# Kernel tuning notes

Measured on AMD Instinct MI355X. Metric: run time of the kernel, lower is better.

The kernel has to match this reference:

```python
import jax, jax.numpy as jnp
import numpy as np

EPS = 1e-8
B, N, W, H = 64, 8192, 64, 4
CTRL = H * (W + 1 + 1 + 3 + 1)  # 280


def setup_inputs() -> dict:
    key = jax.random.key(0)
    k1, k2, k3 = jax.random.split(key, 3)
    memory = jax.random.normal(k1, (B, N, W), dtype=jnp.float32)
    controls = jax.random.normal(k2, (B, CTRL), dtype=jnp.float32)
    prev_weights = jax.random.uniform(k3, (B, H, N), dtype=jnp.float32)
    prev_weights = prev_weights / prev_weights.sum(-1, keepdims=True)
    return {"memory": memory, "controls": controls, "prev_weights": prev_weights}


def reference(memory, controls, prev_weights):
    # memory: [B, N, W]; controls: [B, H*(W+6)]; prev_weights: [B, H, N]
    b, n, w = memory.shape
    h = prev_weights.shape[1]
    # split controls per input_partition = [W, 1, 1, 3, 1] per head
    pos = 0
    keys = controls[:, pos:pos + h * w].reshape(b, h, w); pos += h * w
    betas = controls[:, pos:pos + h].reshape(b, h, 1); pos += h
    gates = controls[:, pos:pos + h].reshape(b, h, 1); pos += h
    shifts = controls[:, pos:pos + 3 * h].reshape(b, h, 3); pos += 3 * h
    gammas = controls[:, pos:pos + h].reshape(b, h, 1)

    keys = jnp.tanh(keys)
    betas = jax.nn.softplus(betas)
    gates = jax.nn.sigmoid(gates)
    shifts = jax.nn.softmax(shifts, axis=-1)
    gammas = 1.0 + jax.nn.softplus(gammas)

    # cosine-similarity content addressing: [B, H, N]
    dots = jnp.einsum('bnw,bhw->bhn', memory, keys)
    norm = (jnp.linalg.norm(keys, axis=-1)[:, :, None]
            * jnp.linalg.norm(memory, axis=-1)[:, None, :])
    scores = dots / (norm + EPS) * betas
    w_content = jax.nn.softmax(scores, axis=-1)

    # interpolate with previous weights
    w_interp = gates * w_content + (1.0 - gates) * prev_weights

    # circular convolution with 3-tap shift kernel (torch conv2d = correlation):
    # out[i] = s0*w[i-1] + s1*w[i] + s2*w[i+1] (indices mod N)
    w_shift = (shifts[..., 0:1] * jnp.roll(w_interp, 1, axis=-1)
               + shifts[..., 1:2] * w_interp
               + shifts[..., 2:3] * jnp.roll(w_interp, -1, axis=-1))

    # sharpen and renormalize
    w_sharp = w_shift ** gammas
    w_sharp = w_sharp / (w_sharp.sum(-1, keepdims=True) + EPS)

    # read: [B, H, W]
    read_data = jnp.einsum('bnw,bhn->bhw', memory, w_sharp)
    return read_data
```

## Files before the change

### kernel.cpp

```cpp
#include <hip/hip_runtime.h>
#include <math.h>

#define B_ 64
#define N_ 8192
#define W_ 64
#define H_ 4
#define CTRL_ 280
#define EPS_ 1e-8f

__device__ __forceinline__ float softplusf(float x) {
    return fmaxf(x, 0.f) + log1pf(expf(-fabsf(x)));
}

__device__ __forceinline__ float waveReduceSum(float v) {
    #pragma unroll
    for (int m = 1; m < 64; m <<= 1) v += __shfl_xor(v, m, 64);
    return v;
}

template <int NW>
__device__ __forceinline__ float blockReduceSum(float v, float* scr) {
    int t = threadIdx.x;
    v = waveReduceSum(v);
    if ((t & 63) == 0) scr[t >> 6] = v;
    __syncthreads();
    float r = 0.f;
    #pragma unroll
    for (int i = 0; i < NW; ++i) r += scr[i];
    __syncthreads();
    return r;
}

__global__ __launch_bounds__(256) void k_scores(const float* __restrict__ mem,
                                                const float* __restrict__ ctrl,
                                                float* __restrict__ expsc) {
    __shared__ float keys[H_ * 68];
    __shared__ float knorm[H_];
    __shared__ float beta[H_];
    __shared__ float sstage[H_ * 65];

    const int t  = threadIdx.x;
    const int b  = blockIdx.y;
    const int n0 = blockIdx.x * 64;

    {
        int h = t >> 6, w = t & 63;
        float kv = tanhf(ctrl[b * CTRL_ + h * W_ + w]);
        keys[h * 68 + w] = kv;
        float ss = waveReduceSum(kv * kv);
        if (w == 0) knorm[h] = sqrtf(ss);
        if (t < H_) beta[t] = softplusf(ctrl[b * CTRL_ + H_ * W_ + t]);
    }
    __syncthreads();

    {
        int row = t >> 2, h = t & 3;
        const float4* mrow = reinterpret_cast<const float4*>(
            mem + ((size_t)b * N_ + n0 + row) * W_);
        const float4* krow = reinterpret_cast<const float4*>(&keys[h * 68]);
        float dot = 0.f, ss = 0.f;
        #pragma unroll
        for (int wg = 0; wg < 16; ++wg) {
            float4 mv = mrow[wg];
            float4 kv = krow[wg];
            dot += mv.x * kv.x + mv.y * kv.y + mv.z * kv.z + mv.w * kv.w;
            ss  += mv.x * mv.x + mv.y * mv.y + mv.z * mv.z + mv.w * mv.w;
        }
        float bh_ = beta[h];
        float sc = dot / (sqrtf(ss) * knorm[h] + EPS_) * bh_;
        sstage[h * 65 + row] = expf(sc - bh_);
    }
    __syncthreads();

    {
        int h = t >> 6, r = t & 63;
        expsc[((size_t)(b * H_ + h)) * N_ + n0 + r] = sstage[h * 65 + r];
    }
}

__global__ __launch_bounds__(512) void k_weights(const float* __restrict__ expsc,
                                                 const float* __restrict__ ctrl,
                                                 const float* __restrict__ prev,
                                                 float* __restrict__ wnorm,
                                                 float* __restrict__ out) {
    __shared__ float scr[8];
    __shared__ float firsts[512];
    __shared__ float lasts[512];

    const int t  = threadIdx.x;
    const int bh = blockIdx.x;
    const int b  = bh >> 2;
    const int h  = bh & 3;

    if (t < 16) {
        float4 z = {0.f, 0.f, 0.f, 0.f};
        reinterpret_cast<float4*>(out + (size_t)bh * 64)[t] = z;
    }

    const float4* sp = reinterpret_cast<const float4*>(expsc + (size_t)bh * N_) + t * 4;
    float a[16];
    float eloc = 0.f;
    #pragma unroll
    for (int i = 0; i < 4; ++i) {
        float4 v = sp[i];
        a[i * 4 + 0] = v.x; a[i * 4 + 1] = v.y; a[i * 4 + 2] = v.z; a[i * 4 + 3] = v.w;
        eloc += v.x + v.y + v.z + v.w;
    }
    float L = blockReduceSum<8>(eloc, scr);
    float invL = 1.f / L;

    const float* cb = ctrl + b * CTRL_;
    float g  = 1.f / (1.f + expf(-cb[260 + h]));
    float r0 = cb[264 + 3 * h], r1 = cb[265 + 3 * h], r2 = cb[266 + 3 * h];
    float rm = fmaxf(r0, fmaxf(r1, r2));
    float e0 = expf(r0 - rm), e1 = expf(r1 - rm), e2 = expf(r2 - rm);
    float ers = 1.f / (e0 + e1 + e2);
    float s0f = e0 * ers, s1f = e1 * ers, s2f = e2 * ers;
    float gamma = 1.f + softplusf(cb[276 + h]);

    const float4* pp = reinterpret_cast<const float4*>(prev + (size_t)bh * N_) + t * 4;
    float wi[16];
    #pragma unroll
    for (int i = 0; i < 4; ++i) {
        float4 v = pp[i];
        wi[i * 4 + 0] = g * (a[i * 4 + 0] * invL) + (1.f - g) * v.x;
        wi[i * 4 + 1] = g * (a[i * 4 + 1] * invL) + (1.f - g) * v.y;
        wi[i * 4 + 2] = g * (a[i * 4 + 2] * invL) + (1.f - g) * v.z;
        wi[i * 4 + 3] = g * (a[i * 4 + 3] * invL) + (1.f - g) * v.w;
    }

    firsts[t] = wi[0];
    lasts[t]  = wi[15];
    __syncthreads();
    float wl = lasts[(t + 511) & 511];
    float wr = firsts[(t + 1) & 511];

    float su = 0.f;
    #pragma unroll
    for (int k = 0; k < 16; ++k) {
        float left  = (k == 0)  ? wl : wi[k - 1];
        float right = (k == 15) ? wr : wi[k + 1];
        float wsv = s0f * left + s1f * wi[k] + s2f * right;
        float uv = powf(wsv, gamma);
        a[k] = uv;
        su += uv;
    }
    float S = blockReduceSum<8>(su, scr);
    float invS = 1.f / (S + EPS_);

    float4* wout = reinterpret_cast<float4*>(wnorm + (size_t)bh * N_) + t * 4;
    #pragma unroll
    for (int i = 0; i < 4; ++i) {
        float4 o;
        o.x = a[i * 4 + 0] * invS; o.y = a[i * 4 + 1] * invS;
        o.z = a[i * 4 + 2] * invS; o.w = a[i * 4 + 3] * invS;
        wout[i] = o;
    }
}

__global__ __launch_bounds__(256) void k_read(const float* __restrict__ mem,
                                              const float* __restrict__ wnorm,
                                              float* __restrict__ out) {
    __shared__ float uLDS[H_ * 256];
    __shared__ float partial[16 * 64];

    const int t  = threadIdx.x;
    const int b  = blockIdx.y;
    const int cb = blockIdx.x * 256;

    {
        int h = t >> 6, i = (t & 63) << 2;
        float4 v = *reinterpret_cast<const float4*>(&wnorm[((size_t)(b * H_ + h)) * N_ + cb + i]);
        *reinterpret_cast<float4*>(&uLDS[h * 256 + i]) = v;
    }
    __syncthreads();

    const int wv = t >> 6, l = t & 63;
    const int rb = wv * 64;
    float acc[4][4] = {};
    const float4* gb = reinterpret_cast<const float4*>(mem + ((size_t)b * N_ + cb) * W_);

    #pragma unroll 4
    for (int it = 0; it < 16; ++it) {
        int r  = rb + it * 4 + (l >> 4);
        float4 mv = gb[(size_t)r * 16 + (l & 15)];
        #pragma unroll
        for (int h = 0; h < 4; ++h) {
            float uh = uLDS[h * 256 + r];
            acc[h][0] += mv.x * uh; acc[h][1] += mv.y * uh;
            acc[h][2] += mv.z * uh; acc[h][3] += mv.w * uh;
        }
    }

    #pragma unroll
    for (int h = 0; h < 4; ++h) {
        #pragma unroll
        for (int j = 0; j < 4; ++j) {
            acc[h][j] += __shfl_xor(acc[h][j], 16, 64);
            acc[h][j] += __shfl_xor(acc[h][j], 32, 64);
        }
    }
    if (l < 16) {
        int c0 = l << 2;
        #pragma unroll
        for (int h = 0; h < 4; ++h)
            #pragma unroll
            for (int j = 0; j < 4; ++j)
                partial[(wv * 4 + h) * 64 + c0 + j] = acc[h][j];
    }
    __syncthreads();

    {
        int h = t >> 6, w = t & 63;
        float sum = partial[(0 * 4 + h) * 64 + w] + partial[(1 * 4 + h) * 64 + w]
                  + partial[(2 * 4 + h) * 64 + w] + partial[(3 * 4 + h) * 64 + w];
        atomicAdd(&out[(size_t)(b * H_ + h) * W_ + w], sum);
    }
}

extern "C" void kernel_launch(void* const* d_in, const int* in_sizes, int n_in,
                              void* d_out, int out_size, void* d_ws, size_t ws_size,
                              hipStream_t stream) {
    const float* mem  = (const float*)d_in[0];
    const float* ctrl = (const float*)d_in[1];
    const float* prev = (const float*)d_in[2];
    float* out = (float*)d_out;

    float* expsc = (float*)d_ws;
    float* wnorm = expsc + (size_t)B_ * H_ * N_;

    k_scores <<<dim3(N_ / 64, B_), 256, 0, stream>>>(mem, ctrl, expsc);
    k_weights<<<dim3(B_ * H_), 512, 0, stream>>>(expsc, ctrl, prev, wnorm, out);
    k_read   <<<dim3(N_ / 256, B_), 256, 0, stream>>>(mem, wnorm, out);
}
```

Before: 238.3 us.

## Fuse weight computation into read kernel with deferred sharpen normalization

```diff
diff --git a/kernel.cpp b/kernel.cpp
--- a/kernel.cpp
+++ b/kernel.cpp
@@ -18,22 +18,10 @@
     return v;
 }
 
-template <int NW>
-__device__ __forceinline__ float blockReduceSum(float v, float* scr) {
-    int t = threadIdx.x;
-    v = waveReduceSum(v);
-    if ((t & 63) == 0) scr[t >> 6] = v;
-    __syncthreads();
-    float r = 0.f;
-    #pragma unroll
-    for (int i = 0; i < NW; ++i) r += scr[i];
-    __syncthreads();
-    return r;
-}
-
 __global__ __launch_bounds__(256) void k_scores(const float* __restrict__ mem,
                                                 const float* __restrict__ ctrl,
-                                                float* __restrict__ expsc) {
+                                                float* __restrict__ e,
+                                                float* __restrict__ L) {
     __shared__ float keys[H_ * 68];
     __shared__ float knorm[H_];
     __shared__ float beta[H_];
@@ -74,108 +62,76 @@
 
     {
         int h = t >> 6, r = t & 63;
-        expsc[((size_t)(b * H_ + h)) * N_ + n0 + r] = sstage[h * 65 + r];
-    }
-}
-
-__global__ __launch_bounds__(512) void k_weights(const float* __restrict__ expsc,
-                                                 const float* __restrict__ ctrl,
-                                                 const float* __restrict__ prev,
-                                                 float* __restrict__ wnorm,
-                                                 float* __restrict__ out) {
-    __shared__ float scr[8];
-    __shared__ float firsts[512];
-    __shared__ float lasts[512];
-
-    const int t  = threadIdx.x;
-    const int bh = blockIdx.x;
-    const int b  = bh >> 2;
-    const int h  = bh & 3;
-
-    if (t < 16) {
-        float4 z = {0.f, 0.f, 0.f, 0.f};
-        reinterpret_cast<float4*>(out + (size_t)bh * 64)[t] = z;
-    }
-
-    const float4* sp = reinterpret_cast<const float4*>(expsc + (size_t)bh * N_) + t * 4;
-    float a[16];
-    float eloc = 0.f;
-    #pragma unroll
-    for (int i = 0; i < 4; ++i) {
-        float4 v = sp[i];
-        a[i * 4 + 0] = v.x; a[i * 4 + 1] = v.y; a[i * 4 + 2] = v.z; a[i * 4 + 3] = v.w;
-        eloc += v.x + v.y + v.z + v.w;
-    }
-    float L = blockReduceSum<8>(eloc, scr);
-    float invL = 1.f / L;
-
-    const float* cb = ctrl + b * CTRL_;
-    float g  = 1.f / (1.f + expf(-cb[260 + h]));
-    float r0 = cb[264 + 3 * h], r1 = cb[265 + 3 * h], r2 = cb[266 + 3 * h];
-    float rm = fmaxf(r0, fmaxf(r1, r2));
-    float e0 = expf(r0 - rm), e1 = expf(r1 - rm), e2 = expf(r2 - rm);
-    float ers = 1.f / (e0 + e1 + e2);
-    float s0f = e0 * ers, s1f = e1 * ers, s2f = e2 * ers;
-    float gamma = 1.f + softplusf(cb[276 + h]);
-
-    const float4* pp = reinterpret_cast<const float4*>(prev + (size_t)bh * N_) + t * 4;
-    float wi[16];
-    #pragma unroll
-    for (int i = 0; i < 4; ++i) {
-        float4 v = pp[i];
-        wi[i * 4 + 0] = g * (a[i * 4 + 0] * invL) + (1.f - g) * v.x;
-        wi[i * 4 + 1] = g * (a[i * 4 + 1] * invL) + (1.f - g) * v.y;
-        wi[i * 4 + 2] = g * (a[i * 4 + 2] * invL) + (1.f - g) * v.z;
-        wi[i * 4 + 3] = g * (a[i * 4 + 3] * invL) + (1.f - g) * v.w;
-    }
-
-    firsts[t] = wi[0];
-    lasts[t]  = wi[15];
-    __syncthreads();
-    float wl = lasts[(t + 511) & 511];
-    float wr = firsts[(t + 1) & 511];
-
-    float su = 0.f;
-    #pragma unroll
-    for (int k = 0; k < 16; ++k) {
-        float left  = (k == 0)  ? wl : wi[k - 1];
-        float right = (k == 15) ? wr : wi[k + 1];
-        float wsv = s0f * left + s1f * wi[k] + s2f * right;
-        float uv = powf(wsv, gamma);
-        a[k] = uv;
-        su += uv;
-    }
-    float S = blockReduceSum<8>(su, scr);
-    float invS = 1.f / (S + EPS_);
-
-    float4* wout = reinterpret_cast<float4*>(wnorm + (size_t)bh * N_) + t * 4;
-    #pragma unroll
-    for (int i = 0; i < 4; ++i) {
-        float4 o;
-        o.x = a[i * 4 + 0] * invS; o.y = a[i * 4 + 1] * invS;
-        o.z = a[i * 4 + 2] * invS; o.w = a[i * 4 + 3] * invS;
-        wout[i] = o;
-    }
-}
-
-__global__ __launch_bounds__(256) void k_read(const float* __restrict__ mem,
-                                              const float* __restrict__ wnorm,
-                                              float* __restrict__ out) {
+        float ev = sstage[h * 65 + r];
+        e[((size_t)(b * H_ + h)) * N_ + n0 + r] = ev;
+        float s = waveReduceSum(ev);
+        if (r == 0) atomicAdd(&L[b * H_ + h], s);
+    }
+}
+
+__global__ __launch_bounds__(256) void k_fused(const float* __restrict__ mem,
+                                               const float* __restrict__ ctrl,
+                                               const float* __restrict__ prev,
+                                               const float* __restrict__ e,
+                                               const float* __restrict__ L,
+                                               float* __restrict__ S,
+                                               float* __restrict__ ounorm) {
     __shared__ float uLDS[H_ * 256];
     __shared__ float partial[16 * 64];
 
     const int t  = threadIdx.x;
     const int b  = blockIdx.y;
     const int cb = blockIdx.x * 256;
-
-    {
-        int h = t >> 6, i = (t & 63) << 2;
-        float4 v = *reinterpret_cast<const float4*>(&wnorm[((size_t)(b * H_ + h)) * N_ + cb + i]);
-        *reinterpret_cast<float4*>(&uLDS[h * 256 + i]) = v;
-    }
-    __syncthreads();
-
     const int wv = t >> 6, l = t & 63;
+
+    {
+        const int h  = wv;
+        const int bh = b * H_ + h;
+        const size_t base = (size_t)bh * N_;
+
+        float4 ev = *reinterpret_cast<const float4*>(e    + base + cb + l * 4);
+        float4 pv = *reinterpret_cast<const float4*>(prev + base + cb + l * 4);
+        float invL = 1.f / L[bh];
+
+        const float* cp = ctrl + b * CTRL_;
+        float g  = 1.f / (1.f + expf(-cp[260 + h]));
+        float r0 = cp[264 + 3 * h], r1 = cp[265 + 3 * h], r2 = cp[266 + 3 * h];
+        float rm = fmaxf(r0, fmaxf(r1, r2));
+        float e0 = expf(r0 - rm), e1 = expf(r1 - rm), e2 = expf(r2 - rm);
+        float ers = 1.f / (e0 + e1 + e2);
+        float s0f = e0 * ers, s1f = e1 * ers, s2f = e2 * ers;
+        float gamma = 1.f + softplusf(cp[276 + h]);
+        float gi = 1.f - g;
+
+        float wi0 = g * (ev.x * invL) + gi * pv.x;
+        float wi1 = g * (ev.y * invL) + gi * pv.y;
+        float wi2 = g * (ev.z * invL) + gi * pv.z;
+        float wi3 = g * (ev.w * invL) + gi * pv.w;
+
+        float wl = __shfl_up(wi3, 1, 64);
+        float wr = __shfl_down(wi0, 1, 64);
+        if (l == 0) {
+            int nl = (cb - 1 + N_) & (N_ - 1);
+            wl = g * (e[base + nl] * invL) + gi * prev[base + nl];
+        }
+        if (l == 63) {
+            int nr = (cb + 256) & (N_ - 1);
+            wr = g * (e[base + nr] * invL) + gi * prev[base + nr];
+        }
+
+        float u0 = powf(s0f * wl  + s1f * wi0 + s2f * wi1, gamma);
+        float u1 = powf(s0f * wi0 + s1f * wi1 + s2f * wi2, gamma);
+        float u2 = powf(s0f * wi1 + s1f * wi2 + s2f * wi3, gamma);
+        float u3 = powf(s0f * wi2 + s1f * wi3 + s2f * wr,  gamma);
+
+        float su = waveReduceSum(u0 + u1 + u2 + u3);
+        if (l == 0) atomicAdd(&S[bh], su);
+
+        float4 uo; uo.x = u0; uo.y = u1; uo.z = u2; uo.w = u3;
+        *reinterpret_cast<float4*>(&uLDS[h * 256 + l * 4]) = uo;
+    }
+    __syncthreads();
+
     const int rb = wv * 64;
     float acc[4][4] = {};
     const float4* gb = reinterpret_cast<const float4*>(mem + ((size_t)b * N_ + cb) * W_);
@@ -214,8 +170,16 @@
         int h = t >> 6, w = t & 63;
         float sum = partial[(0 * 4 + h) * 64 + w] + partial[(1 * 4 + h) * 64 + w]
                   + partial[(2 * 4 + h) * 64 + w] + partial[(3 * 4 + h) * 64 + w];
-        atomicAdd(&out[(size_t)(b * H_ + h) * W_ + w], sum);
-    }
+        atomicAdd(&ounorm[(size_t)(b * H_ + h) * W_ + w], sum);
+    }
+}
+
+__global__ __launch_bounds__(256) void k_final(const float* __restrict__ ounorm,
+                                               const float* __restrict__ S,
+                                               float* __restrict__ out) {
+    int idx = blockIdx.x * 256 + threadIdx.x;
+    int bh  = idx >> 6;
+    out[idx] = ounorm[idx] / (S[bh] + EPS_);
 }
 
 extern "C" void kernel_launch(void* const* d_in, const int* in_sizes, int n_in,
@@ -226,10 +190,13 @@
     const float* prev = (const float*)d_in[2];
     float* out = (float*)d_out;
 
-    float* expsc = (float*)d_ws;
-    float* wnorm = expsc + (size_t)B_ * H_ * N_;
-
-    k_scores <<<dim3(N_ / 64, B_), 256, 0, stream>>>(mem, ctrl, expsc);
-    k_weights<<<dim3(B_ * H_), 512, 0, stream>>>(expsc, ctrl, prev, wnorm, out);
-    k_read   <<<dim3(N_ / 256, B_), 256, 0, stream>>>(mem, wnorm, out);
-}
+    float* e      = (float*)d_ws;
+    float* L      = e + (size_t)B_ * H_ * N_;
+    float* S      = L + B_ * H_;
+    float* ounorm = S + B_ * H_;
+
+    hipMemsetAsync(L, 0, sizeof(float) * (2 * B_ * H_ + B_ * H_ * W_), stream);
+    k_scores<<<dim3(N_ / 64, B_), 256, 0, stream>>>(mem, ctrl, e, L);
+    k_fused <<<dim3(N_ / 256, B_), 256, 0, stream>>>(mem, ctrl, prev, e, L, S, ounorm);
+    k_final <<<dim3(B_ * H_ * W_ / 256), 256, 0, stream>>>(ounorm, S, out);
+}
```

New measurement: 309.4 us. 29.9% more time.
